# Kernel optimization log

Hardware: AMD Instinct MI355X
Metric: run time of the kernel (lower is better)

The kernel has to match this reference:

```python
import jax, jax.numpy as jnp
import numpy as np

B, S, I, H = 128, 1024, 512, 1024


def setup_inputs() -> dict:
    key = jax.random.key(0)
    k0, k1, k2 = jax.random.split(key, 3)
    scale = 0.02
    return {
        "x": jax.random.normal(k0, (B, S, I), jnp.float32),
        "feature_weighting": jnp.ones((1, 1, I), jnp.float32),
        "temporal_weighting": jnp.ones((1, S, 1), jnp.float32),
        "magnitude": jnp.ones((1,), jnp.float32),
        "W0": jax.random.normal(k1, (3 * H, I + H), jnp.float32) * scale,
        "b0": jnp.zeros((3 * H,), jnp.float32),
        "W1": jax.random.normal(k2, (3 * H, 2 * H), jnp.float32) * scale,
        "b1": jnp.zeros((3 * H,), jnp.float32),
    }


def _cell(x_t, h_prev, c_prev, W, b):
    # gates: [B, 3H] from cat(x, h_prev) @ W.T + b
    gates = jnp.concatenate([x_t, h_prev], axis=1) @ W.T + b
    i, g, o = jnp.split(gates, 3, axis=1)
    f = jax.nn.sigmoid(c_prev)            # note: forget gate from c_prev (module's quirk)
    c_new = f * c_prev + jax.nn.sigmoid(i) * jnp.tanh(g)
    h_new = jax.nn.sigmoid(o) * jnp.tanh(c_new) * f  # extra *f (module's quirk)
    return h_new, c_new


def reference(x, feature_weighting, temporal_weighting, magnitude, W0, b0, W1, b1):
    batch = x.shape[0]
    hid = W0.shape[0] // 3
    x = x * feature_weighting * temporal_weighting * jnp.exp(magnitude)
    zeros = jnp.zeros((batch, hid), x.dtype)
    init = (zeros, zeros, zeros, zeros)  # h0, c0, h1, c1

    def step(carry, x_t):
        h0, c0, h1, c1 = carry
        h0, c0 = _cell(x_t, h0, c0, W0, b0)
        h1, c1 = _cell(h0, h1, c1, W1, b1)
        return (h0, c0, h1, c1), h1

    (h0, c0, h1, c1), ys = jax.lax.scan(step, init, jnp.swapaxes(x, 0, 1))
    outputs = jnp.swapaxes(ys, 0, 1)  # [B, S, H]
    return outputs, ((h0, c0), (h1, c1))
```

## Files before the change

### kernel.cpp

```cpp
#include <hip/hip_runtime.h>
#include <hip/hip_bf16.h>


typedef __attribute__((ext_vector_type(8))) _Float16 f16x8;
typedef __attribute__((ext_vector_type(4))) float f32x4;
typedef unsigned long long u64;
#define DEV __device__ __forceinline__

namespace {
constexpr int Bb = 128, Ss = 1024, Ii = 512, Hh = 1024;
constexpr int K0 = Ii + Hh;
constexpr int K1 = 2 * Hh;
constexpr int NWG = 256;
constexpr int NPH = Ss + 1;
constexpr int RING = 16;
constexpr int LAG  = 12;
constexpr int SSTR = 32;

constexpr size_t BH    = (size_t)Bb * Hh;
constexpr size_t OF_H0 = (size_t)Bb * Ss * Hh;
constexpr size_t OF_C0 = OF_H0 + BH;
constexpr size_t OF_H1 = OF_C0 + BH;
constexpr size_t OF_C1 = OF_H1 + BH;

constexpr size_t WS_SLOTS = 4096;
constexpr size_t WS_C0    = 40960;
constexpr size_t WS_C1    = WS_C0 + BH * 4;
constexpr size_t RINGF    = (size_t)RING * BH * 2;
constexpr size_t WS_H0F   = WS_C1 + BH * 4;
constexpr size_t WS_H1F   = WS_H0F + RINGF;
constexpr size_t WS_ZEND  = WS_H1F + RINGF;
constexpr size_t WSZ_W0   = (size_t)3 * Hh * K0 * 2;
constexpr size_t WSZ_W1   = (size_t)3 * Hh * K1 * 2;
constexpr size_t WS_W0F   = WS_ZEND;
constexpr size_t WS_W1F   = WS_W0F + WSZ_W0;
constexpr size_t WS_NEED  = WS_W1F + WSZ_W1;

constexpr int CHUNKB    = 3072;
constexpr int LO_BYTES  = 48 * CHUNKB;
constexpr int RED_BYTES = 4 * 3 * 64 * 16;
constexpr int DYN_LDS   = LO_BYTES + RED_BYTES;
}

DEV unsigned short f16b(float f) {
  return __builtin_bit_cast(unsigned short, (_Float16)f);
}
DEV float sig_(float x) { return 1.f / (1.f + __expf(-x)); }
DEV float tanh_(float x) {
  float e = __expf(-2.f * fabsf(x));
  return copysignf((1.f - e) / (1.f + e), x);
}
DEV f16x8 ldh(const unsigned short* p) { return *reinterpret_cast<const f16x8*>(p); }
#define MFMAH __builtin_amdgcn_mfma_f32_16x16x32_f16

__global__ void k_zero(uint4* p, int n16) {
  for (int i = blockIdx.x * blockDim.x + threadIdx.x; i < n16; i += gridDim.x * blockDim.x)
    p[i] = make_uint4(0u, 0u, 0u, 0u);
}

__global__ void k_convert(const float* __restrict__ W0, const float* __restrict__ W1,
                          unsigned short* __restrict__ w0f, unsigned short* __restrict__ w1f) {
  const long NW04 = (long)3 * Hh * K0 / 4;
  const long NW14 = (long)3 * Hh * K1 / 4;
  const long total = NW04 + NW14;
  for (long i = (long)blockIdx.x * blockDim.x + threadIdx.x; i < total;
       i += (long)gridDim.x * blockDim.x) {
    long e; const float* src; unsigned short* dst;
    if (i < NW04) { e = i * 4;          src = W0 + e; dst = w0f + e; }
    else          { e = (i - NW04) * 4; src = W1 + e; dst = w1f + e; }
    f32x4 v = *(const f32x4*)src;
    u64 pk = 0;
#pragma unroll
    for (int e2 = 0; e2 < 4; ++e2) pk |= (u64)f16b(v[e2]) << (16 * e2);
    *(u64*)dst = pk;
  }
}

#define LD_W(g, kl)                                                           \
  (*(const f16x8*)(lds + ((kl) >> 5) * CHUNKB + (g) * 1024 + l4 * 256 + l15 * 16))

#define HLOAD(arr, n, hP, kaB)                                                \
  _Pragma("unroll") for (int c_ = 0; c_ < (n); ++c_)                          \
    arr[c_] = ldh((hP) + (kaB) + c_ * 32);

#define HCOMP(arr, n, koB)                                                    \
  _Pragma("unroll") for (int c_ = 0; c_ < (n); ++c_) {                        \
    const int ko_ = (koB) + c_ * 32;                                          \
    f32x4 &I_ = (c_ & 1) ? aI1 : aI0;                                         \
    f32x4 &G_ = (c_ & 1) ? aG1 : aG0;                                         \
    f32x4 &O_ = (c_ & 1) ? aO1 : aO0;                                         \
    I_ = MFMAH(LD_W(0, ko_), arr[c_], I_, 0, 0, 0);                           \
    G_ = MFMAH(LD_W(1, ko_), arr[c_], G_, 0, 0, 0);                           \
    O_ = MFMAH(LD_W(2, ko_), arr[c_], O_, 0, 0, 0);                           \
  }

#define WLOAD(a0, a1, a2, n, koB)                                             \
  _Pragma("unroll") for (int c_ = 0; c_ < (n); ++c_) {                        \
    const int ko_ = (koB) + c_ * 32;                                          \
    a0[c_] = ldh(wf + off0 + ko_);                                            \
    a1[c_] = ldh(wf + off1 + ko_);                                            \
    a2[c_] = ldh(wf + off2 + ko_);                                            \
  }

#define GCOMP(h_, a0, a1, a2, n)                                              \
  _Pragma("unroll") for (int c_ = 0; c_ < (n); ++c_) {                        \
    f32x4 &I_ = (c_ & 1) ? aI1 : aI0;                                         \
    f32x4 &G_ = (c_ & 1) ? aG1 : aG0;                                         \
    f32x4 &O_ = (c_ & 1) ? aO1 : aO0;                                         \
    I_ = MFMAH(a0[c_], h_[c_], I_, 0, 0, 0);                                  \
    G_ = MFMAH(a1[c_], h_[c_], G_, 0, 0, 0);                                  \
    O_ = MFMAH(a2[c_], h_[c_], O_, 0, 0, 0);                                  \
  }

#define XCOMP()                                                               \
  _Pragma("unroll") for (int c_ = 0; c_ < 16; ++c_) {                         \
    const int ko_ = c_ * 32;                                                  \
    f32x4 &I_ = (c_ & 1) ? aI1 : aI0;                                         \
    f32x4 &G_ = (c_ & 1) ? aG1 : aG0;                                         \
    f32x4 &O_ = (c_ & 1) ? aO1 : aO0;                                         \
    I_ = MFMAH(LD_W(0, ko_), xp[c_], I_, 0, 0, 0);                            \
    G_ = MFMAH(LD_W(1, ko_), xp[c_], G_, 0, 0, 0);                            \
    O_ = MFMAH(LD_W(2, ko_), xp[c_], O_, 0, 0, 0);                            \
  }

#define XPREF(tn)                                                             \
  do {                                                                        \
    const float* pxn_ = xf + ((size_t)bact * Ss + (tn)) * Ii + l4 * 8;        \
    const float twn_ = tw[tn] * emag;                                         \
    _Pragma("unroll") for (int c_ = 0; c_ < 16; ++c_) {                       \
      const int k_ = c_ * 32;                                                 \
      f32x4 a0_ = *(const f32x4*)(pxn_ + k_);                                 \
      f32x4 a1_ = *(const f32x4*)(pxn_ + k_ + 4);                             \
      f32x4 b0_ = *(const f32x4*)(fw + k_ + l4 * 8);                          \
      f32x4 b1_ = *(const f32x4*)(fw + k_ + l4 * 8 + 4);                      \
      a0_ *= b0_ * twn_; a1_ *= b1_ * twn_;                                   \
      _Pragma("unroll") for (int e_ = 0; e_ < 4; ++e_) {                      \
        xp[c_][e_] = (_Float16)a0_[e_];                                       \
        xp[c_][e_ + 4] = (_Float16)a1_[e_];                                   \
      }                                                                       \
    }                                                                         \
  } while (0)

__global__ __launch_bounds__(512, 1) void lstm_persist(
    const float* __restrict__ xf,
    const float* __restrict__ fw, const float* __restrict__ tw, const float* __restrict__ mag,
    const unsigned short* __restrict__ w0f, const float* __restrict__ b0,
    const unsigned short* __restrict__ w1f, const float* __restrict__ b1,
    float* __restrict__ out,
    unsigned short* __restrict__ h0f, unsigned short* __restrict__ h1f,
    float* __restrict__ c0, float* __restrict__ c1,
    int* __restrict__ slots) {
  extern __shared__ char lds[];
  f32x4* red = reinterpret_cast<f32x4*>(lds + LO_BYTES);

  const int tid = threadIdx.x;
  const int lane = tid & 63;
  const int wv = tid >> 6;
  const int mt = wv & 3;
  const int kh = wv >> 2;
  const int l15 = lane & 15, l4 = lane >> 4;

  const int wg = blockIdx.x;
  const int layer = wg >> 7;
  const int i = wg & 127;
  const int x8 = i & 7;
  const int kk = i >> 3;
  const int mg = x8 >> 2;
  const int jt = (x8 & 3) * 16 + kk;
  const int jb = jt * 16;

  const int dom  = layer * 2 + mg;
  const int pdom = layer ? mg : 2 + mg;
  const int idx  = (x8 & 3) * 16 + kk;

  const int bact = mg * 64 + mt * 16 + l15;
  const int j0 = jb + l4 * 4;
  const bool xwave = (layer == 0) && (kh == 0);

  const int K = layer ? K1 : K0;
  const unsigned short* wf = layer ? w1f : w0f;
  const size_t off0 = (size_t)(0 * Hh + jb + l15) * K + l4 * 8;
  const size_t off1 = (size_t)(1 * Hh + jb + l15) * K + l4 * 8;
  const size_t off2 = (size_t)(2 * Hh + jb + l15) * K + l4 * 8;

  const float* bb = layer ? b1 : b0;
  const f32x4 bi = *(const f32x4*)(bb + j0);
  const f32x4 bg = *(const f32x4*)(bb + Hh + j0);
  const f32x4 bo = *(const f32x4*)(bb + 2 * Hh + j0);

  float* cst = (layer ? c1 : c0) + (size_t)bact * Hh + j0;
  float* outb = out + (size_t)bact * Ss * Hh + j0;
  const float emag = __expf(mag[0]);

  {
    const u64* wsl = (const u64*)wf;
    const int K4 = K >> 2;
    for (int idx2 = tid; idx2 < 48 * 384; idx2 += 512) {
      int R = idx2 / 384;
      int o = idx2 - R * 384;
      int g = R >> 4, rr = R & 15;
      u64 v = wsl[(size_t)(g * Hh + jb + rr) * K4 + o];
      *(u64*)(lds + (o >> 3) * CHUNKB + g * 1024 + ((o >> 1) & 3) * 256 +
              rr * 16 + (o & 1) * 8) = v;
    }
  }
  f16x8 xp[16];
  if (xwave) XPREF(0);
  __syncthreads();

  for (int p = 0; p < NPH; ++p) {
    const bool act = layer ? (p >= 1) : (p < Ss);
    const int t = layer ? (p - 1) : p;
    const int rslot = (p - 1) & (RING - 1);
    const int wslot = p & (RING - 1);

    if (act) {
      f32x4 z = {0.f, 0.f, 0.f, 0.f};
      f32x4 aI0 = z, aG0 = z, aO0 = z, aI1 = z, aG1 = z, aO1 = z;
      const unsigned short* h0r = h0f + (size_t)rslot * BH + (size_t)bact * Hh + l4 * 8;
      const unsigned short* h1r = h1f + (size_t)rslot * BH + (size_t)bact * Hh + l4 * 8;

      if (layer == 0) {
        if (kh == 0) {
          f16x8 hA[8], hB[8];
          HLOAD(hA, 8, h0r, 0);
          HLOAD(hB, 8, h0r, 256);
          XCOMP();
          HCOMP(hA, 8, Ii);
          HCOMP(hB, 8, Ii + 256);
        } else {
          f16x8 hA[8], hB[8];
          HLOAD(hA, 8, h0r, 512);
          HLOAD(hB, 8, h0r, 768);
          HCOMP(hA, 8, Ii + 512);
          HCOMP(hB, 8, Ii + 768);
        }
      } else {
        if (kh == 0) {
          f16x8 g0[12], g1[12], g2a[8], g2b[4], g3[12];
          HLOAD(g0, 12, h0r, 0);
          HLOAD(g1, 12, h0r, 384);
          HCOMP(g0, 12, 0);
          HLOAD(g2a, 8, h0r, 768);
          HLOAD(g2b, 4, h1r, 0);
          HCOMP(g1, 12, 384);
          HLOAD(g3, 12, h1r, 128);
          HCOMP(g2a, 8, 768);
          HCOMP(g2b, 4, Hh);
          HCOMP(g3, 12, Hh + 128);
        } else {
          {
            f16x8 sh[6], sA[6], sB[6], sC[6];
            HLOAD(sh, 6, h1r, 512);
            WLOAD(sA, sB, sC, 6, Hh + 512);
            GCOMP(sh, sA, sB, sC, 6);
          }
          {
            f16x8 sh[6], sA[6], sB[6], sC[6];
            HLOAD(sh, 6, h1r, 704);
            WLOAD(sA, sB, sC, 6, Hh + 704);
            GCOMP(sh, sA, sB, sC, 6);
          }
          {
            f16x8 sh[4], sA[4], sB[4], sC[4];
            HLOAD(sh, 4, h1r, 896);
            WLOAD(sA, sB, sC, 4, Hh + 896);
            GCOMP(sh, sA, sB, sC, 4);
          }
        }
      }

      if (kh == 1) {
        red[((mt * 3 + 0) << 6) + lane] = aI0 + aI1;
        red[((mt * 3 + 1) << 6) + lane] = aG0 + aG1;
        red[((mt * 3 + 2) << 6) + lane] = aO0 + aO1;
      }
      __syncthreads();
      if (kh == 0) {
        f32x4 ai = aI0 + aI1 + red[((mt * 3 + 0) << 6) + lane] + bi;
        f32x4 ag = aG0 + aG1 + red[((mt * 3 + 1) << 6) + lane] + bg;
        f32x4 ao = aO0 + aO1 + red[((mt * 3 + 2) << 6) + lane] + bo;
        f32x4 cp = *(const f32x4*)cst;
        f32x4 cn, hn;
        u64 hpk = 0;
#pragma unroll
        for (int r = 0; r < 4; ++r) {
          float f = sig_(cp[r]);
          float cc = f * cp[r] + sig_(ai[r]) * tanh_(ag[r]);
          float hh = sig_(ao[r]) * tanh_(cc) * f;
          cn[r] = cc; hn[r] = hh;
          hpk |= (u64)f16b(hh) << (16 * r);
        }
        *(f32x4*)cst = cn;
        const size_t wbase = (size_t)wslot * BH + (size_t)bact * Hh + j0;
        __hip_atomic_store((u64*)((layer ? h1f : h0f) + wbase), hpk,
                           __ATOMIC_RELAXED, __HIP_MEMORY_SCOPE_AGENT);
        if (layer) {
          *(f32x4*)(outb + (size_t)t * Hh) = hn;
          if (t == Ss - 1) {
            *(f32x4*)(out + OF_H1 + (size_t)bact * Hh + j0) = hn;
            *(f32x4*)(out + OF_C1 + (size_t)bact * Hh + j0) = cn;
          }
        } else if (t == Ss - 1) {
          *(f32x4*)(out + OF_H0 + (size_t)bact * Hh + j0) = hn;
          *(f32x4*)(out + OF_C0 + (size_t)bact * Hh + j0) = cn;
        }
      }
      if (xwave && t + 1 < Ss) XPREF(t + 1);
    }

    if (p < NPH - 1) {
      __syncthreads();
      if (tid == 0)
        __hip_atomic_store(&slots[(dom * 64 + idx) * SSTR], p + 1,
                           __ATOMIC_RELAXED, __HIP_MEMORY_SCOPE_AGENT);
      const int pthr = layer ? (p + 1) : (p + 1 - LAG);
      bool ok;
      if (tid < 64)        ok = false;
      else if (tid < 128)  ok = (pthr <= 0);
      else                 ok = true;
      int gd = 0;
      do {
        if (!ok) {
          int v = (tid < 64)
              ? __hip_atomic_load(&slots[(dom * 64 + tid) * SSTR],
                                  __ATOMIC_RELAXED, __HIP_MEMORY_SCOPE_AGENT)
              : __hip_atomic_load(&slots[(pdom * 64 + (tid - 64)) * SSTR],
                                  __ATOMIC_RELAXED, __HIP_MEMORY_SCOPE_AGENT);
          ok = v >= ((tid < 64) ? (p + 1) : pthr);
        }
        if (!ok) __builtin_amdgcn_s_sleep(1);
      } while (!__syncthreads_and(ok) && ++gd < (1 << 22));
      if ((p & (RING - 1)) == (RING - 1)) {
        if (tid == 0) __builtin_amdgcn_fence(__ATOMIC_ACQUIRE, "agent");
        __syncthreads();
      }
    }
  }
}

extern "C" void kernel_launch(void* const* d_in, const int* in_sizes, int n_in,
                              void* d_out, int out_size, void* d_ws, size_t ws_size,
                              hipStream_t stream) {
  const float* x   = (const float*)d_in[0];
  const float* fw  = (const float*)d_in[1];
  const float* tw  = (const float*)d_in[2];
  const float* mag = (const float*)d_in[3];
  const float* W0  = (const float*)d_in[4];
  const float* b0  = (const float*)d_in[5];
  const float* W1  = (const float*)d_in[6];
  const float* b1  = (const float*)d_in[7];
  float* out = (float*)d_out;
  char* ws = (char*)d_ws;

  if (ws_size < WS_NEED) return;

  unsigned short* w0f = (unsigned short*)(ws + WS_W0F);
  unsigned short* w1f = (unsigned short*)(ws + WS_W1F);

  (void)hipFuncSetAttribute((const void*)lstm_persist,
                            hipFuncAttributeMaxDynamicSharedMemorySize, DYN_LDS);

  k_zero<<<2048, 256, 0, stream>>>((uint4*)ws, (int)(WS_ZEND / 16));
  k_convert<<<1024, 256, 0, stream>>>(W0, W1, w0f, w1f);

  lstm_persist<<<NWG, 512, DYN_LDS, stream>>>(
      x, fw, tw, mag, w0f, b0, w1f, b1, out,
      (unsigned short*)(ws + WS_H0F), (unsigned short*)(ws + WS_H1F),
      (float*)(ws + WS_C0), (float*)(ws + WS_C1),
      (int*)(ws + WS_SLOTS));
}
```

Baseline: 16.10 ms.

## Precompute input-side gate partials between barriers to shorten the recurrent critical path

Moves the non-recurrent part of each step's gate GEMM off the critical path. Layer 0 now computes the x-projection for step t+1 during the barrier wait, split across both K-half waves. Layer 1 first waits only for the layer-0 domain, computes the h0 contribution, and only then waits for its own h1 peers. The LDS weight cache is rebased so each layer keeps its recurrent slice resident, while layer 1 streams the h0 weights from global memory. This adds register pressure and more global weight traffic on layer 1, and reorders the ring fence relative to the slot publish.

New measurement: 16.17 ms. No clear change (+0.4%).

```diff
diff --git a/kernel.cpp b/kernel.cpp
--- a/kernel.cpp
+++ b/kernel.cpp
@@ -76,22 +76,21 @@
   }
 }
 
-#define LD_W(g, kl)                                                           \
-  (*(const f16x8*)(lds + ((kl) >> 5) * CHUNKB + (g) * 1024 + l4 * 256 + l15 * 16))
+#define LD_WC(g, ch)                                                          \
+  (*(const f16x8*)(lds + (ch) * CHUNKB + (g) * 1024 + l4 * 256 + l15 * 16))
 
 #define HLOAD(arr, n, hP, kaB)                                                \
   _Pragma("unroll") for (int c_ = 0; c_ < (n); ++c_)                          \
     arr[c_] = ldh((hP) + (kaB) + c_ * 32);
 
-#define HCOMP(arr, n, koB)                                                    \
+#define HCOMP(arr, n, cB)                                                     \
   _Pragma("unroll") for (int c_ = 0; c_ < (n); ++c_) {                        \
-    const int ko_ = (koB) + c_ * 32;                                          \
     f32x4 &I_ = (c_ & 1) ? aI1 : aI0;                                         \
     f32x4 &G_ = (c_ & 1) ? aG1 : aG0;                                         \
     f32x4 &O_ = (c_ & 1) ? aO1 : aO0;                                         \
-    I_ = MFMAH(LD_W(0, ko_), arr[c_], I_, 0, 0, 0);                           \
-    G_ = MFMAH(LD_W(1, ko_), arr[c_], G_, 0, 0, 0);                           \
-    O_ = MFMAH(LD_W(2, ko_), arr[c_], O_, 0, 0, 0);                           \
+    I_ = MFMAH(LD_WC(0, (cB) + c_), arr[c_], I_, 0, 0, 0);                    \
+    G_ = MFMAH(LD_WC(1, (cB) + c_), arr[c_], G_, 0, 0, 0);                    \
+    O_ = MFMAH(LD_WC(2, (cB) + c_), arr[c_], O_, 0, 0, 0);                    \
   }
 
 #define WLOAD(a0, a1, a2, n, koB)                                             \
@@ -112,27 +111,16 @@
     O_ = MFMAH(a2[c_], h_[c_], O_, 0, 0, 0);                                  \
   }
 
-#define XCOMP()                                                               \
-  _Pragma("unroll") for (int c_ = 0; c_ < 16; ++c_) {                         \
-    const int ko_ = c_ * 32;                                                  \
-    f32x4 &I_ = (c_ & 1) ? aI1 : aI0;                                         \
-    f32x4 &G_ = (c_ & 1) ? aG1 : aG0;                                         \
-    f32x4 &O_ = (c_ & 1) ? aO1 : aO0;                                         \
-    I_ = MFMAH(LD_W(0, ko_), xp[c_], I_, 0, 0, 0);                            \
-    G_ = MFMAH(LD_W(1, ko_), xp[c_], G_, 0, 0, 0);                            \
-    O_ = MFMAH(LD_W(2, ko_), xp[c_], O_, 0, 0, 0);                            \
-  }
-
-#define XPREF(tn)                                                             \
+#define XPREF8(tn)                                                            \
   do {                                                                        \
-    const float* pxn_ = xf + ((size_t)bact * Ss + (tn)) * Ii + l4 * 8;        \
+    const float* pxn_ = xf + ((size_t)bact * Ss + (tn)) * Ii + khk + l4 * 8;  \
     const float twn_ = tw[tn] * emag;                                         \
-    _Pragma("unroll") for (int c_ = 0; c_ < 16; ++c_) {                       \
+    _Pragma("unroll") for (int c_ = 0; c_ < 8; ++c_) {                        \
       const int k_ = c_ * 32;                                                 \
       f32x4 a0_ = *(const f32x4*)(pxn_ + k_);                                 \
       f32x4 a1_ = *(const f32x4*)(pxn_ + k_ + 4);                             \
-      f32x4 b0_ = *(const f32x4*)(fw + k_ + l4 * 8);                          \
-      f32x4 b1_ = *(const f32x4*)(fw + k_ + l4 * 8 + 4);                      \
+      f32x4 b0_ = *(const f32x4*)(fw + khk + k_ + l4 * 8);                    \
+      f32x4 b1_ = *(const f32x4*)(fw + khk + k_ + l4 * 8 + 4);                \
       a0_ *= b0_ * twn_; a1_ *= b1_ * twn_;                                   \
       _Pragma("unroll") for (int e_ = 0; e_ < 4; ++e_) {                      \
         xp[c_][e_] = (_Float16)a0_[e_];                                       \
@@ -140,6 +128,11 @@
       }                                                                       \
     }                                                                         \
   } while (0)
+
+#define XCOMP8() HCOMP(xp, 8, khc)
+
+#define ZACC() do { f32x4 z_ = {0.f,0.f,0.f,0.f};                             \
+    aI0 = z_; aG0 = z_; aO0 = z_; aI1 = z_; aG1 = z_; aO1 = z_; } while (0)
 
 __global__ __launch_bounds__(512, 1) void lstm_persist(
     const float* __restrict__ xf,
@@ -159,6 +152,8 @@
   const int mt = wv & 3;
   const int kh = wv >> 2;
   const int l15 = lane & 15, l4 = lane >> 4;
+  const int khk = kh * 256;
+  const int khc = kh * 8;
 
   const int wg = blockIdx.x;
   const int layer = wg >> 7;
@@ -175,9 +170,9 @@
 
   const int bact = mg * 64 + mt * 16 + l15;
   const int j0 = jb + l4 * 4;
-  const bool xwave = (layer == 0) && (kh == 0);
 
   const int K = layer ? K1 : K0;
+  const int KB = layer ? 512 : 0;
   const unsigned short* wf = layer ? w1f : w0f;
   const size_t off0 = (size_t)(0 * Hh + jb + l15) * K + l4 * 8;
   const size_t off1 = (size_t)(1 * Hh + jb + l15) * K + l4 * 8;
@@ -195,18 +190,22 @@
   {
     const u64* wsl = (const u64*)wf;
     const int K4 = K >> 2;
-    for (int idx2 = tid; idx2 < 48 * 384; idx2 += 512) {
-      int R = idx2 / 384;
-      int o = idx2 - R * 384;
+    const int cb4 = KB >> 2;
+    for (int q = tid; q < 48 * 384; q += 512) {
+      int R = q / 384;
+      int o = q - R * 384;
       int g = R >> 4, rr = R & 15;
-      u64 v = wsl[(size_t)(g * Hh + jb + rr) * K4 + o];
+      u64 v = wsl[(size_t)(g * Hh + jb + rr) * K4 + cb4 + o];
       *(u64*)(lds + (o >> 3) * CHUNKB + g * 1024 + ((o >> 1) & 3) * 256 +
               rr * 16 + (o & 1) * 8) = v;
     }
   }
-  f16x8 xp[16];
-  if (xwave) XPREF(0);
   __syncthreads();
+
+  f32x4 aI0, aG0, aO0, aI1, aG1, aO1;
+  ZACC();
+  f16x8 xp[8];
+  if (layer == 0) { XPREF8(0); XCOMP8(); }
 
   for (int p = 0; p < NPH; ++p) {
     const bool act = layer ? (p >= 1) : (p < Ss);
@@ -215,59 +214,16 @@
     const int wslot = p & (RING - 1);
 
     if (act) {
-      f32x4 z = {0.f, 0.f, 0.f, 0.f};
-      f32x4 aI0 = z, aG0 = z, aO0 = z, aI1 = z, aG1 = z, aO1 = z;
-      const unsigned short* h0r = h0f + (size_t)rslot * BH + (size_t)bact * Hh + l4 * 8;
-      const unsigned short* h1r = h1f + (size_t)rslot * BH + (size_t)bact * Hh + l4 * 8;
-
-      if (layer == 0) {
-        if (kh == 0) {
-          f16x8 hA[8], hB[8];
-          HLOAD(hA, 8, h0r, 0);
-          HLOAD(hB, 8, h0r, 256);
-          XCOMP();
-          HCOMP(hA, 8, Ii);
-          HCOMP(hB, 8, Ii + 256);
-        } else {
-          f16x8 hA[8], hB[8];
-          HLOAD(hA, 8, h0r, 512);
-          HLOAD(hB, 8, h0r, 768);
-          HCOMP(hA, 8, Ii + 512);
-          HCOMP(hB, 8, Ii + 768);
-        }
+      const unsigned short* hr =
+          (layer ? h1f : h0f) + (size_t)rslot * BH + (size_t)bact * Hh + l4 * 8;
+      if (kh == 0) {
+        f16x8 hA[8], hB[8];
+        HLOAD(hA, 8, hr, 0); HLOAD(hB, 8, hr, 256);
+        HCOMP(hA, 8, 16); HCOMP(hB, 8, 24);
       } else {
-        if (kh == 0) {
-          f16x8 g0[12], g1[12], g2a[8], g2b[4], g3[12];
-          HLOAD(g0, 12, h0r, 0);
-          HLOAD(g1, 12, h0r, 384);
-          HCOMP(g0, 12, 0);
-          HLOAD(g2a, 8, h0r, 768);
-          HLOAD(g2b, 4, h1r, 0);
-          HCOMP(g1, 12, 384);
-          HLOAD(g3, 12, h1r, 128);
-          HCOMP(g2a, 8, 768);
-          HCOMP(g2b, 4, Hh);
-          HCOMP(g3, 12, Hh + 128);
-        } else {
-          {
-            f16x8 sh[6], sA[6], sB[6], sC[6];
-            HLOAD(sh, 6, h1r, 512);
-            WLOAD(sA, sB, sC, 6, Hh + 512);
-            GCOMP(sh, sA, sB, sC, 6);
-          }
-          {
-            f16x8 sh[6], sA[6], sB[6], sC[6];
-            HLOAD(sh, 6, h1r, 704);
-            WLOAD(sA, sB, sC, 6, Hh + 704);
-            GCOMP(sh, sA, sB, sC, 6);
-          }
-          {
-            f16x8 sh[4], sA[4], sB[4], sC[4];
-            HLOAD(sh, 4, h1r, 896);
-            WLOAD(sA, sB, sC, 4, Hh + 896);
-            GCOMP(sh, sA, sB, sC, 4);
-          }
-        }
+        f16x8 hA[8], hB[8];
+        HLOAD(hA, 8, hr, 512); HLOAD(hB, 8, hr, 768);
+        HCOMP(hA, 8, 32); HCOMP(hB, 8, 40);
       }
 
       if (kh == 1) {
@@ -306,34 +262,80 @@
           *(f32x4*)(out + OF_C0 + (size_t)bact * Hh + j0) = cn;
         }
       }
-      if (xwave && t + 1 < Ss) XPREF(t + 1);
     }
 
     if (p < NPH - 1) {
       __syncthreads();
+      if ((p & (RING - 1)) == (RING - 1)) {
+        if (tid == 0) __builtin_amdgcn_fence(__ATOMIC_ACQUIRE, "agent");
+        __syncthreads();
+      }
       if (tid == 0)
         __hip_atomic_store(&slots[(dom * 64 + idx) * SSTR], p + 1,
                            __ATOMIC_RELAXED, __HIP_MEMORY_SCOPE_AGENT);
-      const int pthr = layer ? (p + 1) : (p + 1 - LAG);
-      bool ok;
-      if (tid < 64)        ok = false;
-      else if (tid < 128)  ok = (pthr <= 0);
-      else                 ok = true;
-      int gd = 0;
-      do {
-        if (!ok) {
-          int v = (tid < 64)
-              ? __hip_atomic_load(&slots[(dom * 64 + tid) * SSTR],
-                                  __ATOMIC_RELAXED, __HIP_MEMORY_SCOPE_AGENT)
-              : __hip_atomic_load(&slots[(pdom * 64 + (tid - 64)) * SSTR],
-                                  __ATOMIC_RELAXED, __HIP_MEMORY_SCOPE_AGENT);
-          ok = v >= ((tid < 64) ? (p + 1) : pthr);
+
+      if (layer == 1) {
+        bool ok = (tid >= 64);
+        int gd = 0;
+        do {
+          if (!ok)
+            ok = __hip_atomic_load(&slots[(pdom * 64 + tid) * SSTR],
+                                   __ATOMIC_RELAXED,
+                                   __HIP_MEMORY_SCOPE_AGENT) >= p + 1;
+          if (!ok) __builtin_amdgcn_s_sleep(2);
+        } while (!__syncthreads_and(ok) && ++gd < (1 << 22));
+        ZACC();
+        const unsigned short* h0n =
+            h0f + (size_t)(p & (RING - 1)) * BH + (size_t)bact * Hh + l4 * 8;
+        if (kh == 0) {
+          {
+            f16x8 sh[6], sA[6], sB[6], sC[6];
+            HLOAD(sh, 6, h0n, 0); WLOAD(sA, sB, sC, 6, 0);
+            GCOMP(sh, sA, sB, sC, 6);
+          }
+          {
+            f16x8 sh[6], sA[6], sB[6], sC[6];
+            HLOAD(sh, 6, h0n, 192); WLOAD(sA, sB, sC, 6, 192);
+            GCOMP(sh, sA, sB, sC, 6);
+          }
+          {
+            f16x8 sh[4], sA[4], sB[4], sC[4];
+            HLOAD(sh, 4, h0n, 384); WLOAD(sA, sB, sC, 4, 384);
+            GCOMP(sh, sA, sB, sC, 4);
+          }
+        } else {
+          f16x8 hA[8], hB[8];
+          HLOAD(hA, 8, h0n, 512); HLOAD(hB, 8, h0n, 768);
+          HCOMP(hA, 8, 0); HCOMP(hB, 8, 8);
         }
-        if (!ok) __builtin_amdgcn_s_sleep(1);
-      } while (!__syncthreads_and(ok) && ++gd < (1 << 22));
-      if ((p & (RING - 1)) == (RING - 1)) {
-        if (tid == 0) __builtin_amdgcn_fence(__ATOMIC_ACQUIRE, "agent");
-        __syncthreads();
+        ok = (tid >= 64);
+        gd = 0;
+        do {
+          if (!ok)
+            ok = __hip_atomic_load(&slots[(dom * 64 + tid) * SSTR],
+                                   __ATOMIC_RELAXED,
+                                   __HIP_MEMORY_SCOPE_AGENT) >= p + 1;
+          if (!ok) __builtin_amdgcn_s_sleep(2);
+        } while (!__syncthreads_and(ok) && ++gd < (1 << 22));
+      } else {
+        if (p + 1 < Ss) { XPREF8(p + 1); ZACC(); XCOMP8(); }
+        const int pthr = p + 1 - LAG;
+        bool ok;
+        if (tid < 64)        ok = false;
+        else if (tid < 128)  ok = (pthr <= 0);
+        else                 ok = true;
+        int gd = 0;
+        do {
+          if (!ok) {
+            int v = (tid < 64)
+                ? __hip_atomic_load(&slots[(dom * 64 + tid) * SSTR],
+                                    __ATOMIC_RELAXED, __HIP_MEMORY_SCOPE_AGENT)
+                : __hip_atomic_load(&slots[(pdom * 64 + (tid - 64)) * SSTR],
+                                    __ATOMIC_RELAXED, __HIP_MEMORY_SCOPE_AGENT);
+            ok = v >= ((tid < 64) ? (p + 1) : pthr);
+          }
+          if (!ok) __builtin_amdgcn_s_sleep(2);
+        } while (!__syncthreads_and(ok) && ++gd < (1 << 22));
       }
     }
   }
```
